# Kernel tuning notes

Measured on AMD Instinct MI355X. Metric: run time of the kernel, lower is better.

Reference implementation:

```python
import jax, jax.numpy as jnp
import numpy as np

N = 8192
IN_F = 128
OUT_F = 128


def setup_inputs() -> dict:
    key = jax.random.key(0)
    k1, k2, k3, k4 = jax.random.split(key, 4)
    h = jax.random.normal(k1, (N, IN_F), dtype=jnp.float32)
    pos = jax.random.normal(k2, (N, 1, 3), dtype=jnp.float32)
    # xavier_uniform-ish scale for params
    W = jax.random.uniform(k3, (IN_F, OUT_F), dtype=jnp.float32,
                           minval=-1.0, maxval=1.0) * (1.414 * np.sqrt(6.0 / (IN_F + OUT_F)))
    a = jax.random.uniform(k4, (2 * OUT_F + 3, 1), dtype=jnp.float32,
                           minval=-1.0, maxval=1.0) * (1.414 * np.sqrt(6.0 / (2 * OUT_F + 3 + 1)))
    return {"h": h, "pos": pos, "W": W, "a": a}


def reference(h, pos, W, a):
    # Wh: [N, F]
    Wh = h @ W
    F_ = Wh.shape[1]
    a1 = a[:F_, 0]          # weights on Wh[j] (the repeated / neighbor features)
    a2 = a[F_:2 * F_, 0]    # weights on Wh[i] (the repeat_interleaved / center features)
    a3 = a[2 * F_:, 0]      # weights on pos[i] - pos[j]
    p = pos.reshape(-1, 3)  # [N, 3]
    s_j = Wh @ a1           # [N]
    s_i = Wh @ a2           # [N]
    p_a = p @ a3            # [N]
    # e[i, j] = leaky_relu(Wh[j].a1 + Wh[i].a2 + (pos[i]-pos[j]).a3)
    e = jax.nn.leaky_relu(s_i[:, None] + s_j[None, :] + p_a[:, None] - p_a[None, :],
                          negative_slope=0.2)  # [N, N]
    attention = jax.nn.softmax(e, axis=1)
    # eval mode: dropout is identity
    h_prime = attention @ Wh  # [N, F]
    return jax.nn.elu(h_prime)
```

## Files before the change

kernel.cpp:

```cpp
#include <hip/hip_runtime.h>
#include <hip/hip_bf16.h>

#define N 8192
#define F 128
#define JC 8
#define JSLICE (N / JC)

typedef __attribute__((ext_vector_type(4)))  float f32x4;
typedef __attribute__((ext_vector_type(16))) float f32x16;
typedef __attribute__((ext_vector_type(8)))  short short8;

static __device__ __forceinline__ short bf16bits(float x) {
  __hip_bfloat16 b = __float2bfloat16(x);
  return *reinterpret_cast<short*>(&b);
}

__global__ __launch_bounds__(256) void k_gemm_cd(
    const float* __restrict__ h, const float* __restrict__ pos,
    const float* __restrict__ W, const float* __restrict__ a,
    unsigned short* __restrict__ WhTf, float* __restrict__ cArr,
    float* __restrict__ dArr)
{
  __shared__ float Ws[128 * 128];
  const int tid = threadIdx.x;
  const int r0  = blockIdx.x * 16;

  {
    f32x4* Ws4 = (f32x4*)Ws;
    const f32x4* Wg4 = (const f32x4*)W;
#pragma unroll
    for (int q = 0; q < 16; ++q) Ws4[q * 256 + tid] = Wg4[q * 256 + tid];
  }
  __syncthreads();

  const int rg  = tid >> 5;
  const int c32 = tid & 31;

  f32x4 acc0, acc1;
#pragma unroll
  for (int i = 0; i < 4; ++i) { acc0[i] = 0.0f; acc1[i] = 0.0f; }

  const f32x4* h40 = (const f32x4*)(h + (size_t)(r0 + rg * 2) * 128);
  const f32x4* h41 = (const f32x4*)(h + (size_t)(r0 + rg * 2 + 1) * 128);
  const f32x4* Ws4 = (const f32x4*)Ws;

#pragma unroll 4
  for (int k4 = 0; k4 < 32; ++k4) {
    f32x4 hv0 = h40[k4];
    f32x4 hv1 = h41[k4];
#pragma unroll
    for (int e = 0; e < 4; ++e) {
      f32x4 w = Ws4[(k4 * 4 + e) * 32 + c32];
      acc0 += hv0[e] * w;
      acc1 += hv1[e] * w;
    }
  }

  f32x4 a1v = *(const f32x4*)(a + c32 * 4);
  f32x4 a2v = *(const f32x4*)(a + 128 + c32 * 4);
#pragma unroll
  for (int rr = 0; rr < 2; ++rr) {
    f32x4 accR = rr ? acc1 : acc0;
    f32x4 t1 = accR * a1v;
    f32x4 t2 = accR * a2v;
    float s1 = t1[0] + t1[1] + t1[2] + t1[3];
    float s2 = t2[0] + t2[1] + t2[2] + t2[3];
#pragma unroll
    for (int m = 1; m < 32; m <<= 1) {
      s1 += __shfl_xor(s1, m);
      s2 += __shfl_xor(s2, m);
    }
    if (c32 == 0) {
      const int row = r0 + rg * 2 + rr;
      float pa = pos[row * 3 + 0] * a[256] + pos[row * 3 + 1] * a[257] +
                 pos[row * 3 + 2] * a[258];
      cArr[row] = s2 + pa;
      dArr[row] = s1 - pa;
    }
  }

  __syncthreads();
  float* tmp = Ws;
  {
    const int base = (rg * 2) * 132 + c32 * 4;
    *(f32x4*)&tmp[base]       = acc0;
    *(f32x4*)&tmp[base + 132] = acc1;
  }
  __syncthreads();
  {
    const int col  = tid >> 1;
    const int half = tid & 1;
    short8 o;
#pragma unroll
    for (int rr = 0; rr < 8; ++rr)
      o[rr] = bf16bits(tmp[(half * 8 + rr) * 132 + col]);
    *(short8*)(WhTf + (size_t)(r0 >> 4) * 2048 + col * 16 + half * 8) = o;
  }
}

__global__ __launch_bounds__(256, 4) void k_flash(
    const unsigned short* __restrict__ WhTf, const float* __restrict__ cArr,
    const float* __restrict__ dArr, float* __restrict__ pnum,
    float* __restrict__ pden)
{
  __shared__ __align__(16) float dS[JSLICE];
  __shared__ float red[64 * 128];
  __shared__ float denS[64];

  const int tid = threadIdx.x;
  const int jc  = blockIdx.x >> 7;
  const int r0  = (blockIdx.x & 127) * 64;

  {
    const f32x4* s4 = (const f32x4*)(dArr + (size_t)jc * JSLICE);
    ((f32x4*)dS)[tid] = s4[tid];
  }
  __syncthreads();

  const int w  = tid >> 6;
  const int l  = tid & 63;
  const int cl = l & 31;
  const int kh = l >> 5;
  const int rt = w & 1;
  const int jw = (w >> 1) * (JSLICE / 2);
  const float L2E = 1.44269504f;
  const float ci = cArr[r0 + rt * 32 + cl] * L2E;

  f32x16 acc0, acc1, acc2, acc3;
#pragma unroll
  for (int i = 0; i < 16; ++i) { acc0[i] = 0; acc1[i] = 0; acc2[i] = 0; acc3[i] = 0; }
  float den = 0.0f;

  const unsigned short* bPtr =
      WhTf + ((size_t)(jc * JSLICE + jw) >> 4) * 2048 + cl * 16 + kh * 8;
  const float* dPtr = dS + jw + kh * 8;

  short8 b0 = *(const short8*)(bPtr);
  short8 b1 = *(const short8*)(bPtr + 512);
  short8 b2 = *(const short8*)(bPtr + 1024);
  short8 b3 = *(const short8*)(bPtr + 1536);
  bPtr += 2048;

  const int iters = (JSLICE / 2) / 16;
  for (int kk = 0; kk < iters; ++kk) {
    short8 n0 = *(const short8*)(bPtr);
    short8 n1 = *(const short8*)(bPtr + 512);
    short8 n2 = *(const short8*)(bPtr + 1024);
    short8 n3 = *(const short8*)(bPtr + 1536);

    f32x4 dj0 = *(const f32x4*)(dPtr);
    f32x4 dj1 = *(const f32x4*)(dPtr + 4);
    short8 af;
#pragma unroll
    for (int e = 0; e < 8; ++e) {
      float dj = (e < 4) ? dj0[e] : dj1[e - 4];
      float u = __builtin_fmaf(dj, L2E, ci);
      u = fmaxf(u, 0.2f * u);
      float pv = __builtin_amdgcn_exp2f(u);
      den += pv;
      af[e] = bf16bits(pv);
    }

    acc0 = __builtin_amdgcn_mfma_f32_32x32x16_bf16(af, b0, acc0, 0, 0, 0);
    acc1 = __builtin_amdgcn_mfma_f32_32x32x16_bf16(af, b1, acc1, 0, 0, 0);
    acc2 = __builtin_amdgcn_mfma_f32_32x32x16_bf16(af, b2, acc2, 0, 0, 0);
    acc3 = __builtin_amdgcn_mfma_f32_32x32x16_bf16(af, b3, acc3, 0, 0, 0);

    b0 = n0; b1 = n1; b2 = n2; b3 = n3;
    bPtr += 2048; dPtr += 16;
  }

  den += __shfl_xor(den, 32);

  const int rtb = 32 * rt;
  const int rhi = 4 * kh;
  if (w < 2) {
#pragma unroll
    for (int reg = 0; reg < 16; ++reg) {
      const int rr = (reg & 3) + 8 * (reg >> 2) + rhi;
      red[(rtb + rr) * 128 +  0 + cl] = acc0[reg];
      red[(rtb + rr) * 128 + 32 + cl] = acc1[reg];
      red[(rtb + rr) * 128 + 64 + cl] = acc2[reg];
      red[(rtb + rr) * 128 + 96 + cl] = acc3[reg];
    }
    if (l < 32) denS[rtb + l] = den;
  }
  __syncthreads();
  if (w >= 2) {
#pragma unroll
    for (int reg = 0; reg < 16; ++reg) {
      const int rr = (reg & 3) + 8 * (reg >> 2) + rhi;
      red[(rtb + rr) * 128 +  0 + cl] += acc0[reg];
      red[(rtb + rr) * 128 + 32 + cl] += acc1[reg];
      red[(rtb + rr) * 128 + 64 + cl] += acc2[reg];
      red[(rtb + rr) * 128 + 96 + cl] += acc3[reg];
    }
    if (l < 32) denS[rtb + l] += den;
  }
  __syncthreads();

  {
    f32x4* pn4 = (f32x4*)(pnum + (size_t)jc * N * F + (size_t)r0 * 128);
    const f32x4* r4 = (const f32x4*)red;
#pragma unroll
    for (int q = 0; q < 8; ++q) pn4[q * 256 + tid] = r4[q * 256 + tid];
    if (tid < 64) pden[(size_t)jc * N + r0 + tid] = denS[tid];
  }
}

__global__ __launch_bounds__(256) void k_final(
    const float* __restrict__ pnum, const float* __restrict__ pden,
    float* __restrict__ out)
{
  const int g = blockIdx.x * 256 + threadIdx.x;
  const int row = g >> 5;
  f32x4 n;
#pragma unroll
  for (int i = 0; i < 4; ++i) n[i] = 0.0f;
  float dd = 0.0f;
#pragma unroll
  for (int c = 0; c < JC; ++c) {
    n += ((const f32x4*)pnum)[(size_t)c * (N * F / 4) + g];
    dd += pden[(size_t)c * N + row];
  }
  f32x4 r = n * (1.0f / dd);
#pragma unroll
  for (int i = 0; i < 4; ++i) {
    float x = r[i];
    r[i] = x > 0.0f ? x : (__builtin_amdgcn_exp2f(x * 1.44269504f) - 1.0f);
  }
  ((f32x4*)out)[g] = r;
}

extern "C" void kernel_launch(void* const* d_in, const int* in_sizes, int n_in,
                              void* d_out, int out_size, void* d_ws, size_t ws_size,
                              hipStream_t stream)
{
  const float* h   = (const float*)d_in[0];
  const float* pos = (const float*)d_in[1];
  const float* W   = (const float*)d_in[2];
  const float* a   = (const float*)d_in[3];
  float* out = (float*)d_out;

  char* ws = (char*)d_ws;
  unsigned short* WhTf = (unsigned short*)ws;
  float* cArr = (float*)(ws + (size_t)2 * 1024 * 1024);
  float* dArr = cArr + N;
  float* pden = dArr + N;
  float* pnum = pden + (size_t)JC * N;

  hipLaunchKernelGGL(k_gemm_cd, dim3(512), dim3(256), 0, stream,
                     h, pos, W, a, WhTf, cArr, dArr);
  hipLaunchKernelGGL(k_flash, dim3(128 * JC), dim3(256), 0, stream,
                     WhTf, cArr, dArr, pnum, pden);
  hipLaunchKernelGGL(k_final, dim3((N * F / 4) / 256), dim3(256), 0, stream,
                     pnum, pden, out);
}
```

Before: 111.1 us.

## Stage Wh tiles in LDS via async loads, 128-row blocks sharing B

The flash kernel now has each block cover 128 rows, one 32-row tile per wave, over a 512-column j-slice. The bf16 Wh tiles are double-buffered in LDS using global_load_lds, so all four waves reuse the same B operand instead of each loading it from global memory. The intra-block split-K reduction through LDS is removed, and each wave writes its partial numerator and denominator straight to global. JC doubles to 16, so the partial buffers and k_final's reduction pass grow twofold, and the chunk loop adds a barrier per 32-column chunk.

```diff
diff --git a/kernel.cpp b/kernel.cpp
--- a/kernel.cpp
+++ b/kernel.cpp
@@ -3,8 +3,10 @@
 
 #define N 8192
 #define F 128
-#define JC 8
+#define JC 16
 #define JSLICE (N / JC)
+#define CHUNKJ 32
+#define NSC (JSLICE / CHUNKJ)
 
 typedef __attribute__((ext_vector_type(4)))  float f32x4;
 typedef __attribute__((ext_vector_type(16))) float f32x16;
@@ -13,6 +15,12 @@
 static __device__ __forceinline__ short bf16bits(float x) {
   __hip_bfloat16 b = __float2bfloat16(x);
   return *reinterpret_cast<short*>(&b);
+}
+
+static __device__ __forceinline__ void gload_lds16(const void* g, void* lds) {
+  __builtin_amdgcn_global_load_lds(
+      (const __attribute__((address_space(1))) void*)g,
+      (__attribute__((address_space(3))) void*)lds, 16, 0, 0);
 }
 
 __global__ __launch_bounds__(256) void k_gemm_cd(
@@ -103,108 +111,95 @@
     const float* __restrict__ dArr, float* __restrict__ pnum,
     float* __restrict__ pden)
 {
+  __shared__ __align__(16) unsigned short bufS[2][CHUNKJ * 128];
   __shared__ __align__(16) float dS[JSLICE];
-  __shared__ float red[64 * 128];
-  __shared__ float denS[64];
 
   const int tid = threadIdx.x;
-  const int jc  = blockIdx.x >> 7;
-  const int r0  = (blockIdx.x & 127) * 64;
-
-  {
-    const f32x4* s4 = (const f32x4*)(dArr + (size_t)jc * JSLICE);
-    ((f32x4*)dS)[tid] = s4[tid];
-  }
-  __syncthreads();
+  const int rb  = blockIdx.x & 63;
+  const int jc  = blockIdx.x >> 6;
+  const int r0  = rb * 128;
 
   const int w  = tid >> 6;
   const int l  = tid & 63;
   const int cl = l & 31;
   const int kh = l >> 5;
-  const int rt = w & 1;
-  const int jw = (w >> 1) * (JSLICE / 2);
+
+  const unsigned short* gBase = WhTf + ((size_t)jc * 32) * 2048;
+
+  {
+    const char* gs = (const char*)gBase + (w * 2) * 1024 + l * 16;
+    char* ld = (char*)&bufS[0][0] + (w * 2) * 1024;
+    gload_lds16(gs, ld);
+    gload_lds16(gs + 1024, ld + 1024);
+    if (tid < JSLICE / 4)
+      ((f32x4*)dS)[tid] = ((const f32x4*)(dArr + (size_t)jc * JSLICE))[tid];
+  }
+  __syncthreads();
+
   const float L2E = 1.44269504f;
-  const float ci = cArr[r0 + rt * 32 + cl] * L2E;
+  const float ci = cArr[r0 + w * 32 + cl] * L2E;
 
   f32x16 acc0, acc1, acc2, acc3;
 #pragma unroll
   for (int i = 0; i < 16; ++i) { acc0[i] = 0; acc1[i] = 0; acc2[i] = 0; acc3[i] = 0; }
-  float den = 0.0f;
-
-  const unsigned short* bPtr =
-      WhTf + ((size_t)(jc * JSLICE + jw) >> 4) * 2048 + cl * 16 + kh * 8;
-  const float* dPtr = dS + jw + kh * 8;
-
-  short8 b0 = *(const short8*)(bPtr);
-  short8 b1 = *(const short8*)(bPtr + 512);
-  short8 b2 = *(const short8*)(bPtr + 1024);
-  short8 b3 = *(const short8*)(bPtr + 1536);
-  bPtr += 2048;
-
-  const int iters = (JSLICE / 2) / 16;
-  for (int kk = 0; kk < iters; ++kk) {
-    short8 n0 = *(const short8*)(bPtr);
-    short8 n1 = *(const short8*)(bPtr + 512);
-    short8 n2 = *(const short8*)(bPtr + 1024);
-    short8 n3 = *(const short8*)(bPtr + 1536);
-
-    f32x4 dj0 = *(const f32x4*)(dPtr);
-    f32x4 dj1 = *(const f32x4*)(dPtr + 4);
-    short8 af;
-#pragma unroll
-    for (int e = 0; e < 8; ++e) {
-      float dj = (e < 4) ? dj0[e] : dj1[e - 4];
-      float u = __builtin_fmaf(dj, L2E, ci);
-      u = fmaxf(u, 0.2f * u);
-      float pv = __builtin_amdgcn_exp2f(u);
-      den += pv;
-      af[e] = bf16bits(pv);
-    }
-
-    acc0 = __builtin_amdgcn_mfma_f32_32x32x16_bf16(af, b0, acc0, 0, 0, 0);
-    acc1 = __builtin_amdgcn_mfma_f32_32x32x16_bf16(af, b1, acc1, 0, 0, 0);
-    acc2 = __builtin_amdgcn_mfma_f32_32x32x16_bf16(af, b2, acc2, 0, 0, 0);
-    acc3 = __builtin_amdgcn_mfma_f32_32x32x16_bf16(af, b3, acc3, 0, 0, 0);
-
-    b0 = n0; b1 = n1; b2 = n2; b3 = n3;
-    bPtr += 2048; dPtr += 16;
-  }
-
+  float denA = 0.0f, denB = 0.0f;
+
+  for (int sc = 0; sc < NSC; ++sc) {
+    const int cur = sc & 1;
+    if (sc + 1 < NSC) {
+      const char* gs = (const char*)gBase + (size_t)(sc + 1) * (CHUNKJ * 128 * 2)
+                     + (w * 2) * 1024 + l * 16;
+      char* ld = (char*)&bufS[cur ^ 1][0] + (w * 2) * 1024;
+      gload_lds16(gs, ld);
+      gload_lds16(gs + 1024, ld + 1024);
+    }
+
+#pragma unroll
+    for (int ks = 0; ks < 2; ++ks) {
+      const unsigned short* bs = &bufS[cur][ks * 2048];
+      short8 b0 = *(const short8*)(bs +    0 + cl * 16 + kh * 8);
+      short8 b1 = *(const short8*)(bs +  512 + cl * 16 + kh * 8);
+      short8 b2 = *(const short8*)(bs + 1024 + cl * 16 + kh * 8);
+      short8 b3 = *(const short8*)(bs + 1536 + cl * 16 + kh * 8);
+
+      const int jo = sc * CHUNKJ + ks * 16 + kh * 8;
+      f32x4 dj0 = *(const f32x4*)&dS[jo];
+      f32x4 dj1 = *(const f32x4*)&dS[jo + 4];
+
+      short8 af;
+#pragma unroll
+      for (int e = 0; e < 8; ++e) {
+        float dj = (e < 4) ? dj0[e] : dj1[e - 4];
+        float u = __builtin_fmaf(dj, L2E, ci);
+        u = fmaxf(u, 0.2f * u);
+        float pv = __builtin_amdgcn_exp2f(u);
+        if (e & 1) denB += pv; else denA += pv;
+        af[e] = bf16bits(pv);
+      }
+
+      acc0 = __builtin_amdgcn_mfma_f32_32x32x16_bf16(af, b0, acc0, 0, 0, 0);
+      acc1 = __builtin_amdgcn_mfma_f32_32x32x16_bf16(af, b1, acc1, 0, 0, 0);
+      acc2 = __builtin_amdgcn_mfma_f32_32x32x16_bf16(af, b2, acc2, 0, 0, 0);
+      acc3 = __builtin_amdgcn_mfma_f32_32x32x16_bf16(af, b3, acc3, 0, 0, 0);
+    }
+    __syncthreads();
+  }
+
+  float den = denA + denB;
   den += __shfl_xor(den, 32);
 
-  const int rtb = 32 * rt;
-  const int rhi = 4 * kh;
-  if (w < 2) {
+  {
+    float* base = pnum + (size_t)jc * N * F + (size_t)(r0 + w * 32) * 128;
 #pragma unroll
     for (int reg = 0; reg < 16; ++reg) {
-      const int rr = (reg & 3) + 8 * (reg >> 2) + rhi;
-      red[(rtb + rr) * 128 +  0 + cl] = acc0[reg];
-      red[(rtb + rr) * 128 + 32 + cl] = acc1[reg];
-      red[(rtb + rr) * 128 + 64 + cl] = acc2[reg];
-      red[(rtb + rr) * 128 + 96 + cl] = acc3[reg];
-    }
-    if (l < 32) denS[rtb + l] = den;
-  }
-  __syncthreads();
-  if (w >= 2) {
-#pragma unroll
-    for (int reg = 0; reg < 16; ++reg) {
-      const int rr = (reg & 3) + 8 * (reg >> 2) + rhi;
-      red[(rtb + rr) * 128 +  0 + cl] += acc0[reg];
-      red[(rtb + rr) * 128 + 32 + cl] += acc1[reg];
-      red[(rtb + rr) * 128 + 64 + cl] += acc2[reg];
-      red[(rtb + rr) * 128 + 96 + cl] += acc3[reg];
-    }
-    if (l < 32) denS[rtb + l] += den;
-  }
-  __syncthreads();
-
-  {
-    f32x4* pn4 = (f32x4*)(pnum + (size_t)jc * N * F + (size_t)r0 * 128);
-    const f32x4* r4 = (const f32x4*)red;
-#pragma unroll
-    for (int q = 0; q < 8; ++q) pn4[q * 256 + tid] = r4[q * 256 + tid];
-    if (tid < 64) pden[(size_t)jc * N + r0 + tid] = denS[tid];
+      const int row = (reg & 3) + 8 * (reg >> 2) + 4 * kh;
+      float* rp = base + row * 128 + cl;
+      rp[0]  = acc0[reg];
+      rp[32] = acc1[reg];
+      rp[64] = acc2[reg];
+      rp[96] = acc3[reg];
+    }
+    if (l < 32) pden[(size_t)jc * N + r0 + w * 32 + l] = den;
   }
 }
 
@@ -251,7 +246,7 @@
 
   hipLaunchKernelGGL(k_gemm_cd, dim3(512), dim3(256), 0, stream,
                      h, pos, W, a, WhTf, cArr, dArr);
-  hipLaunchKernelGGL(k_flash, dim3(128 * JC), dim3(256), 0, stream,
+  hipLaunchKernelGGL(k_flash, dim3(64 * JC), dim3(256), 0, stream,
                      WhTf, cArr, dArr, pnum, pden);
   hipLaunchKernelGGL(k_final, dim3((N * F / 4) / 256), dim3(256), 0, stream,
                      pnum, pden, out);
```

After: 109.6 us. Within noise of the previous version (-1.3%).
